# Kernel tuning notes

Hardware: AMD Instinct MI355X
Metric: run time of the kernel (lower is better)

Reference implementation:

```python
import jax, jax.numpy as jnp
import numpy as np

IN_DIM = 768
ATT_DIM = 512
N_HEADS = 8
HEAD_DIM = ATT_DIM // N_HEADS


def setup_inputs() -> dict:
    key = jax.random.key(0)
    k1, k2, k3 = jax.random.split(key, 3)
    X = jax.random.normal(k1, (4, 2048, IN_DIM), dtype=jnp.float32)
    # qkv linear (no bias): weight [3*att_dim, in_dim], torch convention y = x W^T
    W_qkv = jax.random.normal(k2, (3 * ATT_DIM, IN_DIM), dtype=jnp.float32) * (1.0 / np.sqrt(IN_DIM))
    W_out = jax.random.normal(k3, (IN_DIM, ATT_DIM), dtype=jnp.float32) * (1.0 / np.sqrt(ATT_DIM))
    b_out = jnp.zeros((IN_DIM,), dtype=jnp.float32)
    return {"X": X, "W_qkv": W_qkv, "W_out": W_out, "b_out": b_out}


def reference(X, W_qkv, W_out, b_out):
    b, n, _ = X.shape
    QKV = jnp.einsum('bnf,cf->bnc', X, W_qkv)  # [b, n, 3*att_dim]
    # rearrange 'b n (p h d) -> p b h n d'
    QKV = QKV.reshape(b, n, 3, N_HEADS, HEAD_DIM).transpose(2, 0, 3, 1, 4)
    Q, K, V = QKV[0], QKV[1], QKV[2]  # each [b, h, n, d]
    scores = jnp.einsum('bhid,bhjd->bhij', Q, K) / np.sqrt(HEAD_DIM)
    A = jax.nn.softmax(scores, axis=-1)  # dropout p=0 -> identity
    Y = jnp.einsum('bhij,bhjd->bhid', A, V)
    Y = Y.transpose(0, 2, 1, 3).reshape(b, n, ATT_DIM)  # 'b h n d -> b n (h d)'
    return jnp.einsum('bna,oa->bno', Y, W_out) + b_out
```

## Files before the change

kernel.cpp:

```cpp
#include <hip/hip_runtime.h>

typedef __bf16 bf16;
typedef unsigned int u32;
typedef __attribute__((ext_vector_type(8))) __bf16 bf16x8;
typedef __attribute__((ext_vector_type(4))) __bf16 bf16x4;
typedef __attribute__((ext_vector_type(4))) float floatx4;
typedef __attribute__((ext_vector_type(16))) float floatx16;
typedef __attribute__((ext_vector_type(4))) int int4v;

#define IN_DIM  768
#define ATT_DIM 512
#define NH      8
#define HD      64
#define BATCH   4
#define SEQ     2048
#define M_TOT   (BATCH*SEQ)
#define QKV_N   (3*ATT_DIM)

#define QSCALE 0.18033688011112042f

__device__ __forceinline__ void cp16(void* lds, const void* g) {
    __builtin_amdgcn_global_load_lds((const __attribute__((address_space(1))) u32*)g,
                                     (__attribute__((address_space(3))) u32*)lds, 16, 0, 0);
}
__device__ __forceinline__ const bf16* swz(const bf16* b, int row, int chunk) {
    return b + row * 64 + (((chunk) ^ (row & 7)) << 3);
}

__device__ __forceinline__ int cvtpk_bf16(float lo, float hi) {
    int r;
    asm("v_cvt_pk_bf16_f32 %0, %1, %2" : "=v"(r) : "v"(lo), "v"(hi));
    return r;
}
__device__ __forceinline__ void plswap(int& a, int& b) {
    asm("v_permlane32_swap_b32 %0, %1" : "+v"(a), "+v"(b));
}

#define N8_X  (M_TOT * IN_DIM / 8)
#define N8_WQ (QKV_N * IN_DIM / 8)
#define N8_WO (IN_DIM * ATT_DIM / 8)
#define N8_ALL (N8_X + N8_WQ + N8_WO)

__global__ __launch_bounds__(256) void cvt_all(const float* __restrict__ X,
                                               const float* __restrict__ Wq,
                                               const float* __restrict__ Wo,
                                               bf16* __restrict__ Xb,
                                               bf16* __restrict__ Wqb,
                                               bf16* __restrict__ Wob) {
    int i = blockIdx.x * 256 + threadIdx.x;
    const float* s; bf16* d; int off;
    if (i < N8_X)            { s = X;  d = Xb;  off = i; }
    else if (i < N8_X+N8_WQ) { s = Wq; d = Wqb; off = i - N8_X; }
    else                     { s = Wo; d = Wob; off = i - N8_X - N8_WQ; }
    const float4 a = ((const float4*)s)[2*off];
    const float4 b = ((const float4*)s)[2*off+1];
    bf16x8 o = {(bf16)a.x,(bf16)a.y,(bf16)a.z,(bf16)a.w,
                (bf16)b.x,(bf16)b.y,(bf16)b.z,(bf16)b.w};
    ((bf16x8*)d)[off] = o;
}

__global__ __launch_bounds__(256) void qkv_gemm(const bf16* __restrict__ Xb,
                                                const bf16* __restrict__ Wb,
                                                bf16* __restrict__ Q,
                                                bf16* __restrict__ Kv,
                                                bf16* __restrict__ VT) {
    __shared__ __align__(16) char smraw[65536];
    bf16* As = (bf16*)smraw;
    bf16* Bs = (bf16*)(smraw + 32768);

    const int tid  = threadIdx.x;
    const int id  = blockIdx.y * 12 + blockIdx.x;
    const int nid = (id & 7) * 96 + (id >> 3);
    const int bm0 = (nid / 12) * 128;
    const int bn0 = (nid % 12) * 128;
    const int wave = tid >> 6, lane = tid & 63;
    const int quad = lane >> 4, l15 = lane & 15;
    const int wm = (wave >> 1) * 64, wn = (wave & 1) * 64;
    const int r8 = lane >> 3, cc = (lane & 7) ^ r8;

    const bf16* ag = Xb + (size_t)(bm0 + wave * 32 + r8) * IN_DIM + cc * 8;
    const bf16* bg = Wb + (size_t)(bn0 + wave * 32 + r8) * IN_DIM + cc * 8;

    floatx4 acc[4][4];
#pragma unroll
    for (int i = 0; i < 4; ++i)
#pragma unroll
        for (int j = 0; j < 4; ++j) acc[i][j] = (floatx4){0.f, 0.f, 0.f, 0.f};

#pragma unroll
    for (int it = 0; it < 4; ++it) {
        cp16(&As[(wave * 32 + it * 8) * 64], ag + it * (8 * IN_DIM));
        cp16(&Bs[(wave * 32 + it * 8) * 64], bg + it * (8 * IN_DIM));
    }

    for (int kt = 0; kt < IN_DIM / 64; ++kt) {
        const int cur = kt & 1;
        const bf16* Ac = As + cur * 8192;
        const bf16* Bc = Bs + cur * 8192;
        __syncthreads();
        if (kt < IN_DIM / 64 - 1) {
            bf16* An = As + (cur ^ 1) * 8192;
            bf16* Bn = Bs + (cur ^ 1) * 8192;
#pragma unroll
            for (int it = 0; it < 4; ++it) {
                cp16(&An[(wave * 32 + it * 8) * 64],
                     ag + it * (8 * IN_DIM) + (kt + 1) * 64);
                cp16(&Bn[(wave * 32 + it * 8) * 64],
                     bg + it * (8 * IN_DIM) + (kt + 1) * 64);
            }
        }

        bf16x8 af[2][4], bfr[2][4];
#pragma unroll
        for (int kh = 0; kh < 2; ++kh)
#pragma unroll
            for (int i = 0; i < 4; ++i) {
                af[kh][i]  = *(const bf16x8*)swz(Ac, wm + i * 16 + l15, kh * 4 + quad);
                bfr[kh][i] = *(const bf16x8*)swz(Bc, wn + i * 16 + l15, kh * 4 + quad);
            }
#pragma unroll
        for (int kh = 0; kh < 2; ++kh)
#pragma unroll
            for (int i = 0; i < 4; ++i)
#pragma unroll
                for (int j = 0; j < 4; ++j)
                    acc[i][j] = __builtin_amdgcn_mfma_f32_16x16x32_bf16(af[kh][i], bfr[kh][j], acc[i][j], 0, 0, 0);
    }

    const int b = bm0 >> 11, nbase = bm0 & 2047;

    if (bn0 < 512) {
#pragma unroll
        for (int i = 0; i < 4; ++i)
#pragma unroll
            for (int j = 0; j < 4; ++j)
#pragma unroll
                for (int r = 0; r < 4; ++r) {
                    const int row = bm0 + wm + i * 16 + quad * 4 + r;
                    const int col = bn0 + wn + j * 16 + l15;
                    const int h = col >> 6, d = col & 63;
                    const int n = row & 2047;
                    const size_t idx = (((size_t)((row >> 11) * NH + h)) * SEQ + n) * HD + d;
                    Q[idx] = (bf16)(acc[i][j][r] * QSCALE);
                }
    } else if (bn0 < 1024) {
#pragma unroll
        for (int i = 0; i < 4; ++i)
#pragma unroll
            for (int j = 0; j < 4; ++j)
#pragma unroll
                for (int r = 0; r < 4; ++r) {
                    const int row = bm0 + wm + i * 16 + quad * 4 + r;
                    const int col = bn0 - 512 + wn + j * 16 + l15;
                    const int h = col >> 6, d = col & 63;
                    const int n = row & 2047;
                    const size_t idx = (((size_t)((row >> 11) * NH + h)) * SEQ + n) * HD + d;
                    Kv[idx] = (bf16)acc[i][j][r];
                }
    } else {
        __syncthreads();
        bf16 (*Ts)[136] = (bf16(*)[136])smraw;
#pragma unroll
        for (int i = 0; i < 4; ++i)
#pragma unroll
            for (int j = 0; j < 4; ++j) {
                bf16x4 pk = {(bf16)acc[i][j][0], (bf16)acc[i][j][1],
                             (bf16)acc[i][j][2], (bf16)acc[i][j][3]};
                *(bf16x4*)&Ts[wn + j * 16 + l15][wm + i * 16 + quad * 4] = pk;
            }
        __syncthreads();
        const int cb = bn0 - 1024;
#pragma unroll
        for (int t2 = 0; t2 < 8; ++t2) {
            const int id2 = tid + t2 * 256;
            const int c = id2 >> 4, nc = (id2 & 15) * 8;
            const int col = cb + c;
            const int h = col >> 6, d = col & 63;
            *(bf16x8*)&VT[(((size_t)(b * NH + h)) * HD + d) * SEQ + nbase + nc] =
                *(const bf16x8*)&Ts[c][nc];
        }
    }
}

__global__ __launch_bounds__(256, 4) void attn(const bf16* __restrict__ Q,
                                               const bf16* __restrict__ K,
                                               const bf16* __restrict__ VT,
                                               bf16* __restrict__ Y) {
    __shared__ bf16 Ks[2][64 * 64];
    __shared__ bf16 VTs[2][64 * 64];

    const int tid  = threadIdx.x;
    const int wave = tid >> 6, lane = tid & 63;
    const int l31  = lane & 31, hi = lane >> 5;
    const int bh = blockIdx.x;
    const int q0 = blockIdx.y * 128;
    const bf16* Qg = Q  + (size_t)bh * SEQ * HD;
    const bf16* Kg = K  + (size_t)bh * SEQ * HD;
    const bf16* Vg = VT + (size_t)bh * HD * SEQ;

    bf16x8 aq[4];
    {
        const bf16* qrow = Qg + (size_t)(q0 + wave * 32 + l31) * HD;
#pragma unroll
        for (int c = 0; c < 4; ++c)
            aq[c] = *(const bf16x8*)(qrow + c * 16 + hi * 8);
    }

    const int r8 = lane >> 3, cc8 = (lane & 7) ^ r8;
    const bf16* kgw = Kg + (size_t)(wave * 16 + r8) * HD + cc8 * 8;
    const bf16* vgw = Vg + (size_t)(wave * 16 + r8) * SEQ + cc8 * 8;

    float l = 0.f;
    floatx16 o[2];
#pragma unroll
    for (int i = 0; i < 16; ++i) { o[0][i] = 0.f; o[1][i] = 0.f; }

#pragma unroll
    for (int it = 0; it < 2; ++it) {
        cp16(&Ks[0][(wave * 16 + it * 8) * 64], kgw + (size_t)(it * 8) * HD);
        cp16(&VTs[0][(wave * 16 + it * 8) * 64], vgw + (size_t)(it * 8) * SEQ);
    }

    for (int kt = 0; kt < SEQ / 64; ++kt) {
        const int cur = kt & 1;
        __syncthreads();
        if (kt < SEQ / 64 - 1) {
#pragma unroll
            for (int it = 0; it < 2; ++it) {
                cp16(&Ks[cur ^ 1][(wave * 16 + it * 8) * 64],
                     kgw + (size_t)((kt + 1) * 64 + it * 8) * HD);
                cp16(&VTs[cur ^ 1][(wave * 16 + it * 8) * 64],
                     vgw + (size_t)(it * 8) * SEQ + (kt + 1) * 64);
            }
        }

#pragma unroll
        for (int kb = 0; kb < 2; ++kb) {
            const int krow = kb * 32 + l31;
            floatx16 s;
#pragma unroll
            for (int i = 0; i < 16; ++i) s[i] = 0.f;
#pragma unroll
            for (int c = 0; c < 4; ++c) {
                const bf16x8 kf = *(const bf16x8*)swz(Ks[cur], krow, c * 2 + hi);
                s = __builtin_amdgcn_mfma_f32_32x32x16_bf16(kf, aq[c], s, 0, 0, 0);
            }
            float p[16];
#pragma unroll
            for (int i = 0; i < 16; ++i) p[i] = __builtin_amdgcn_exp2f(s[i]);
            {
                const float t0 = (p[0] + p[1]) + (p[2] + p[3]);
                const float t1 = (p[4] + p[5]) + (p[6] + p[7]);
                const float t2 = (p[8] + p[9]) + (p[10] + p[11]);
                const float t3 = (p[12] + p[13]) + (p[14] + p[15]);
                l += (t0 + t1) + (t2 + t3);
            }
            int w[8];
#pragma unroll
            for (int i = 0; i < 8; ++i) w[i] = cvtpk_bf16(p[2 * i], p[2 * i + 1]);
            plswap(w[0], w[2]); plswap(w[1], w[3]);
            plswap(w[4], w[6]); plswap(w[5], w[7]);
            const int4v f0i = {w[0], w[1], w[2], w[3]};
            const int4v f1i = {w[4], w[5], w[6], w[7]};
            const bf16x8 f0 = __builtin_bit_cast(bf16x8, f0i);
            const bf16x8 f1 = __builtin_bit_cast(bf16x8, f1i);
#pragma unroll
            for (int db = 0; db < 2; ++db) {
                const int vrow = db * 32 + l31;
                const bf16x8 v0 = *(const bf16x8*)swz(VTs[cur], vrow, kb * 4 + hi);
                const bf16x8 v1 = *(const bf16x8*)swz(VTs[cur], vrow, kb * 4 + 2 + hi);
                o[db] = __builtin_amdgcn_mfma_f32_32x32x16_bf16(f0, v0, o[db], 0, 0, 0);
                o[db] = __builtin_amdgcn_mfma_f32_32x32x16_bf16(f1, v1, o[db], 0, 0, 0);
            }
        }
    }

    l += __shfl_xor(l, 32, 64);
    const float inv = 1.0f / l;
    const int b = bh >> 3, h = bh & 7;
#pragma unroll
    for (int reg = 0; reg < 16; ++reg) {
        const int qr = (reg & 3) + 8 * (reg >> 2) + 4 * hi;
        const float li = __int_as_float(
            __builtin_amdgcn_ds_bpermute(qr << 2, __float_as_int(inv)));
        const int n = q0 + wave * 32 + qr;
        bf16* yrow = Y + ((size_t)(b * SEQ + n)) * ATT_DIM + h * HD + l31;
        yrow[0]  = (bf16)(o[0][reg] * li);
        yrow[32] = (bf16)(o[1][reg] * li);
    }
}

__global__ __launch_bounds__(256) void out_gemm(const bf16* __restrict__ Yb,
                                                const bf16* __restrict__ Wb,
                                                const float* __restrict__ bias,
                                                float* __restrict__ out) {
    __shared__ __align__(16) char smraw[65536];
    bf16* As = (bf16*)smraw;
    bf16* Bs = (bf16*)(smraw + 32768);

    const int tid  = threadIdx.x;
    const int id  = blockIdx.y * 6 + blockIdx.x;
    const int nid = (id & 7) * 48 + (id >> 3);
    const int bm0 = (nid / 6) * 128;
    const int bn0 = (nid % 6) * 128;
    const int wave = tid >> 6, lane = tid & 63;
    const int quad = lane >> 4, l15 = lane & 15;
    const int wm = (wave >> 1) * 64, wn = (wave & 1) * 64;
    const int r8 = lane >> 3, cc = (lane & 7) ^ r8;

    const bf16* ag = Yb + (size_t)(bm0 + wave * 32 + r8) * ATT_DIM + cc * 8;
    const bf16* bg = Wb + (size_t)(bn0 + wave * 32 + r8) * ATT_DIM + cc * 8;

    floatx4 acc[4][4];
#pragma unroll
    for (int i = 0; i < 4; ++i)
#pragma unroll
        for (int j = 0; j < 4; ++j) acc[i][j] = (floatx4){0.f, 0.f, 0.f, 0.f};

#pragma unroll
    for (int it = 0; it < 4; ++it) {
        cp16(&As[(wave * 32 + it * 8) * 64], ag + it * (8 * ATT_DIM));
        cp16(&Bs[(wave * 32 + it * 8) * 64], bg + it * (8 * ATT_DIM));
    }

    for (int kt = 0; kt < ATT_DIM / 64; ++kt) {
        const int cur = kt & 1;
        const bf16* Ac = As + cur * 8192;
        const bf16* Bc = Bs + cur * 8192;
        __syncthreads();
        if (kt < ATT_DIM / 64 - 1) {
            bf16* An = As + (cur ^ 1) * 8192;
            bf16* Bn = Bs + (cur ^ 1) * 8192;
#pragma unroll
            for (int it = 0; it < 4; ++it) {
                cp16(&An[(wave * 32 + it * 8) * 64],
                     ag + it * (8 * ATT_DIM) + (kt + 1) * 64);
                cp16(&Bn[(wave * 32 + it * 8) * 64],
                     bg + it * (8 * ATT_DIM) + (kt + 1) * 64);
            }
        }

        bf16x8 af[2][4], bfr[2][4];
#pragma unroll
        for (int kh = 0; kh < 2; ++kh)
#pragma unroll
            for (int i = 0; i < 4; ++i) {
                af[kh][i]  = *(const bf16x8*)swz(Ac, wm + i * 16 + l15, kh * 4 + quad);
                bfr[kh][i] = *(const bf16x8*)swz(Bc, wn + i * 16 + l15, kh * 4 + quad);
            }
#pragma unroll
        for (int kh = 0; kh < 2; ++kh)
#pragma unroll
            for (int i = 0; i < 4; ++i)
#pragma unroll
                for (int j = 0; j < 4; ++j)
                    acc[i][j] = __builtin_amdgcn_mfma_f32_16x16x32_bf16(af[kh][i], bfr[kh][j], acc[i][j], 0, 0, 0);
    }

#pragma unroll
    for (int i = 0; i < 4; ++i)
#pragma unroll
        for (int j = 0; j < 4; ++j)
#pragma unroll
            for (int r = 0; r < 4; ++r) {
                const int row = bm0 + wm + i * 16 + quad * 4 + r;
                const int col = bn0 + wn + j * 16 + l15;
                out[(size_t)row * IN_DIM + col] = acc[i][j][r] + bias[col];
            }
}

extern "C" void kernel_launch(void* const* d_in, const int* in_sizes, int n_in,
                              void* d_out, int out_size, void* d_ws, size_t ws_size,
                              hipStream_t stream) {
    const float* X    = (const float*)d_in[0];
    const float* Wqkv = (const float*)d_in[1];
    const float* Wout = (const float*)d_in[2];
    const float* bout = (const float*)d_in[3];
    float* out = (float*)d_out;

    char* ws = (char*)d_ws;
    size_t off = 0;
    bf16* Xb  = (bf16*)(ws + off); off += (size_t)M_TOT * IN_DIM * 2;
    bf16* Wqb = (bf16*)(ws + off); off += (size_t)QKV_N * IN_DIM * 2;
    bf16* Wob = (bf16*)(ws + off); off += (size_t)IN_DIM * ATT_DIM * 2;
    const size_t T = (size_t)BATCH * NH * SEQ * HD * 2;
    bf16* Q  = (bf16*)(ws + off); off += T;
    bf16* K  = (bf16*)(ws + off); off += T;
    bf16* VT = (bf16*)(ws + off); off += T;
    bf16* Y  = (bf16*)(ws + off); off += T;

    cvt_all<<<N8_ALL / 256, 256, 0, stream>>>(X, Wqkv, Wout, Xb, Wqb, Wob);
    qkv_gemm<<<dim3(QKV_N / 128, M_TOT / 128), 256, 0, stream>>>(Xb, Wqb, Q, K, VT);
    attn<<<dim3(BATCH * NH, SEQ / 128), 256, 0, stream>>>(Q, K, VT, Y);
    out_gemm<<<dim3(IN_DIM / 128, M_TOT / 128), 256, 0, stream>>>(Y, Wob, bout, out);
}
```

Baseline: 159.0 us.

## Restructure QKV GEMM to two waves with 64x128 warp tiles, single-buffered LDS

The QKV projection GEMM now runs with 128 threads (2 waves) per 128x128 block instead of 4. Each wave computes a 64x128 sub-tile with 32 accumulators, which raises MFMA work per LDS fragment load. The double-buffered async prefetch is replaced by a single LDS buffer filled and consumed between two barriers, and the shared memory footprint shrinks. The trade-off is fewer waves to hide latency, no overlap of the global loads with compute, and higher register pressure.

Result: slower. 163.7 us (+2.9%).

```diff
diff --git a/kernel.cpp b/kernel.cpp
--- a/kernel.cpp
+++ b/kernel.cpp
@@ -59,14 +59,14 @@
     ((bf16x8*)d)[off] = o;
 }
 
-__global__ __launch_bounds__(256) void qkv_gemm(const bf16* __restrict__ Xb,
-                                                const bf16* __restrict__ Wb,
-                                                bf16* __restrict__ Q,
-                                                bf16* __restrict__ Kv,
-                                                bf16* __restrict__ VT) {
-    __shared__ __align__(16) char smraw[65536];
+__global__ __launch_bounds__(128, 2) void qkv_gemm(const bf16* __restrict__ Xb,
+                                                   const bf16* __restrict__ Wb,
+                                                   bf16* __restrict__ Q,
+                                                   bf16* __restrict__ Kv,
+                                                   bf16* __restrict__ VT) {
+    __shared__ __align__(16) char smraw[36864];
     bf16* As = (bf16*)smraw;
-    bf16* Bs = (bf16*)(smraw + 32768);
+    bf16* Bs = (bf16*)(smraw + 16384);
 
     const int tid  = threadIdx.x;
     const int id  = blockIdx.y * 12 + blockIdx.x;
@@ -75,56 +75,42 @@
     const int bn0 = (nid % 12) * 128;
     const int wave = tid >> 6, lane = tid & 63;
     const int quad = lane >> 4, l15 = lane & 15;
-    const int wm = (wave >> 1) * 64, wn = (wave & 1) * 64;
+    const int wm = wave * 64;
     const int r8 = lane >> 3, cc = (lane & 7) ^ r8;
 
-    const bf16* ag = Xb + (size_t)(bm0 + wave * 32 + r8) * IN_DIM + cc * 8;
-    const bf16* bg = Wb + (size_t)(bn0 + wave * 32 + r8) * IN_DIM + cc * 8;
-
-    floatx4 acc[4][4];
+    const bf16* ag = Xb + (size_t)(bm0 + wm + r8) * IN_DIM + cc * 8;
+    const bf16* bg = Wb + (size_t)(bn0 + wm + r8) * IN_DIM + cc * 8;
+
+    floatx4 acc[4][8];
 #pragma unroll
     for (int i = 0; i < 4; ++i)
 #pragma unroll
-        for (int j = 0; j < 4; ++j) acc[i][j] = (floatx4){0.f, 0.f, 0.f, 0.f};
-
-#pragma unroll
-    for (int it = 0; it < 4; ++it) {
-        cp16(&As[(wave * 32 + it * 8) * 64], ag + it * (8 * IN_DIM));
-        cp16(&Bs[(wave * 32 + it * 8) * 64], bg + it * (8 * IN_DIM));
-    }
+        for (int j = 0; j < 8; ++j) acc[i][j] = (floatx4){0.f, 0.f, 0.f, 0.f};
 
     for (int kt = 0; kt < IN_DIM / 64; ++kt) {
-        const int cur = kt & 1;
-        const bf16* Ac = As + cur * 8192;
-        const bf16* Bc = Bs + cur * 8192;
-        __syncthreads();
-        if (kt < IN_DIM / 64 - 1) {
-            bf16* An = As + (cur ^ 1) * 8192;
-            bf16* Bn = Bs + (cur ^ 1) * 8192;
-#pragma unroll
-            for (int it = 0; it < 4; ++it) {
-                cp16(&An[(wave * 32 + it * 8) * 64],
-                     ag + it * (8 * IN_DIM) + (kt + 1) * 64);
-                cp16(&Bn[(wave * 32 + it * 8) * 64],
-                     bg + it * (8 * IN_DIM) + (kt + 1) * 64);
-            }
-        }
-
-        bf16x8 af[2][4], bfr[2][4];
-#pragma unroll
-        for (int kh = 0; kh < 2; ++kh)
-#pragma unroll
-            for (int i = 0; i < 4; ++i) {
-                af[kh][i]  = *(const bf16x8*)swz(Ac, wm + i * 16 + l15, kh * 4 + quad);
-                bfr[kh][i] = *(const bf16x8*)swz(Bc, wn + i * 16 + l15, kh * 4 + quad);
-            }
-#pragma unroll
-        for (int kh = 0; kh < 2; ++kh)
+        __syncthreads();
+#pragma unroll
+        for (int it = 0; it < 8; ++it) {
+            cp16(&As[(wm + it * 8) * 64], ag + it * (8 * IN_DIM) + kt * 64);
+            cp16(&Bs[(wm + it * 8) * 64], bg + it * (8 * IN_DIM) + kt * 64);
+        }
+        __syncthreads();
+
+#pragma unroll
+        for (int kh = 0; kh < 2; ++kh) {
+            bf16x8 af[4], bfr[8];
 #pragma unroll
             for (int i = 0; i < 4; ++i)
-#pragma unroll
-                for (int j = 0; j < 4; ++j)
-                    acc[i][j] = __builtin_amdgcn_mfma_f32_16x16x32_bf16(af[kh][i], bfr[kh][j], acc[i][j], 0, 0, 0);
+                af[i] = *(const bf16x8*)swz(As, wm + i * 16 + l15, kh * 4 + quad);
+#pragma unroll
+            for (int j = 0; j < 8; ++j)
+                bfr[j] = *(const bf16x8*)swz(Bs, j * 16 + l15, kh * 4 + quad);
+#pragma unroll
+            for (int i = 0; i < 4; ++i)
+#pragma unroll
+                for (int j = 0; j < 8; ++j)
+                    acc[i][j] = __builtin_amdgcn_mfma_f32_16x16x32_bf16(af[i], bfr[j], acc[i][j], 0, 0, 0);
+        }
     }
 
     const int b = bm0 >> 11, nbase = bm0 & 2047;
@@ -133,11 +119,11 @@
 #pragma unroll
         for (int i = 0; i < 4; ++i)
 #pragma unroll
-            for (int j = 0; j < 4; ++j)
+            for (int j = 0; j < 8; ++j)
 #pragma unroll
                 for (int r = 0; r < 4; ++r) {
                     const int row = bm0 + wm + i * 16 + quad * 4 + r;
-                    const int col = bn0 + wn + j * 16 + l15;
+                    const int col = bn0 + j * 16 + l15;
                     const int h = col >> 6, d = col & 63;
                     const int n = row & 2047;
                     const size_t idx = (((size_t)((row >> 11) * NH + h)) * SEQ + n) * HD + d;
@@ -147,11 +133,11 @@
 #pragma unroll
         for (int i = 0; i < 4; ++i)
 #pragma unroll
-            for (int j = 0; j < 4; ++j)
+            for (int j = 0; j < 8; ++j)
 #pragma unroll
                 for (int r = 0; r < 4; ++r) {
                     const int row = bm0 + wm + i * 16 + quad * 4 + r;
-                    const int col = bn0 - 512 + wn + j * 16 + l15;
+                    const int col = bn0 - 512 + j * 16 + l15;
                     const int h = col >> 6, d = col & 63;
                     const int n = row & 2047;
                     const size_t idx = (((size_t)((row >> 11) * NH + h)) * SEQ + n) * HD + d;
@@ -163,16 +149,16 @@
 #pragma unroll
         for (int i = 0; i < 4; ++i)
 #pragma unroll
-            for (int j = 0; j < 4; ++j) {
+            for (int j = 0; j < 8; ++j) {
                 bf16x4 pk = {(bf16)acc[i][j][0], (bf16)acc[i][j][1],
                              (bf16)acc[i][j][2], (bf16)acc[i][j][3]};
-                *(bf16x4*)&Ts[wn + j * 16 + l15][wm + i * 16 + quad * 4] = pk;
+                *(bf16x4*)&Ts[j * 16 + l15][wm + i * 16 + quad * 4] = pk;
             }
         __syncthreads();
         const int cb = bn0 - 1024;
 #pragma unroll
-        for (int t2 = 0; t2 < 8; ++t2) {
-            const int id2 = tid + t2 * 256;
+        for (int t2 = 0; t2 < 16; ++t2) {
+            const int id2 = tid + t2 * 128;
             const int c = id2 >> 4, nc = (id2 & 15) * 8;
             const int col = cb + c;
             const int h = col >> 6, d = col & 63;
@@ -390,7 +376,7 @@
     bf16* Y  = (bf16*)(ws + off); off += T;
 
     cvt_all<<<N8_ALL / 256, 256, 0, stream>>>(X, Wqkv, Wout, Xb, Wqb, Wob);
-    qkv_gemm<<<dim3(QKV_N / 128, M_TOT / 128), 256, 0, stream>>>(Xb, Wqb, Q, K, VT);
+    qkv_gemm<<<dim3(QKV_N / 128, M_TOT / 128), 128, 0, stream>>>(Xb, Wqb, Q, K, VT);
     attn<<<dim3(BATCH * NH, SEQ / 128), 256, 0, stream>>>(Q, K, VT, Y);
     out_gemm<<<dim3(IN_DIM / 128, M_TOT / 128), 256, 0, stream>>>(Y, Wob, bout, out);
 }
```
